# Optimization experiments

Measured on AMD Instinct MI355X. Metric: run time of the kernel, lower is better.

Reference implementation:

```python
import jax, jax.numpy as jnp
import numpy as np

N, C_IN, C_OUT, T, V = 64, 64, 64, 300, 25


def setup_inputs() -> dict:
    key = jax.random.key(0)
    k1, k2, k3, k4 = jax.random.split(key, 4)
    x = jax.random.normal(k1, (N, C_IN, T, V), dtype=jnp.float32)
    a = jax.random.uniform(k2, (N, T, V, V), dtype=jnp.float32)
    # 1x1 Conv2D (channels_first) == per-pixel channel-mixing matmul
    W = jax.random.normal(k3, (C_IN, C_OUT), dtype=jnp.float32) * (1.0 / np.sqrt(C_IN))
    b = jax.random.normal(k4, (C_OUT,), dtype=jnp.float32) * 0.01
    return {"x": x, "a": a, "W": W, "b": b}


def reference(x, a, W, b):
    # 1x1 conv channels_first: mix channels at every (t, v) location
    y = jnp.einsum('nctv,cd->ndtv', x, W) + b[None, :, None, None]
    # dropout in eval mode (training=False) is identity
    # spatial graph convolution: node mixing with per-(n,t) adjacency
    out = jnp.einsum('nctv,ntvw->nctw', y, a)
    return (out, a)
```

## Files before the change

kernel.cpp:

```cpp
#include <hip/hip_runtime.h>


typedef __attribute__((ext_vector_type(8))) short short8;
typedef __attribute__((ext_vector_type(4))) float f32x4;

#define XS_S 66
#define YS_S 36
#define AT_S 36

__device__ __forceinline__ unsigned short f2bf(float f) {
    unsigned int u = __builtin_bit_cast(unsigned int, f);
    return (unsigned short)((u + 0x7FFFu + ((u >> 16) & 1u)) >> 16);
}

__global__ __launch_bounds__(512, 6)
void sgcn_fused(const float* __restrict__ xg, const float* __restrict__ ag,
                const float* __restrict__ Wg, const float* __restrict__ bg,
                float* __restrict__ outg)
{
    __shared__ alignas(16) unsigned short Wt[64 * XS_S];
    __shared__ alignas(16) unsigned short Xs[4][32 * XS_S];
    __shared__ alignas(16) unsigned short Ys[8][32 * YS_S];
    __shared__ alignas(16) unsigned short At[4][32 * AT_S];

    const int tid  = threadIdx.x;
    const int wid  = tid >> 6;
    const int lane = tid & 63;
    const int q    = lane >> 4;
    const int lo   = lane & 15;

    const int bid = blockIdx.x;
    const int n   = bid / 75;
    const int t0  = (bid % 75) * 4;

    f32x4 xv[4];
    const long xbase = ((long)n * 64 * 300 + t0) * 25;
#pragma unroll
    for (int m = 0; m < 4; ++m) {
        const int f = tid + 512 * m;
        if (m < 3 || f < 1600) {
            const int c = f / 25, j = f % 25;
            xv[m] = *(const f32x4*)(xg + xbase + (long)c * 7500 + 4 * j);
        }
    }
    f32x4 av[2];
    const long abase = ((long)n * 300 + t0) * 625;
#pragma unroll
    for (int m = 0; m < 2; ++m) {
        const int f = tid + 512 * m;
        if (m < 1 || f < 625)
            av[m] = *(const f32x4*)(ag + abase + 4 * f);
    }
    f32x4 wv[2];
#pragma unroll
    for (int m = 0; m < 2; ++m)
        wv[m] = *(const f32x4*)(Wg + 4 * (tid + 512 * m));

    if (tid < 256) {
        unsigned short* yr = &Ys[tid >> 5][(tid & 31) * YS_S];
#pragma unroll
        for (int i = 25; i < 32; ++i) yr[i] = 0;
    } else if (tid < 384) {
        const int r = tid - 256;
        unsigned short* ar = &At[r >> 5][(r & 31) * AT_S];
#pragma unroll
        for (int i = 25; i < 32; ++i) ar[i] = 0;
    }

#pragma unroll
    for (int m = 0; m < 2; ++m) {
        const int f = 4 * (tid + 512 * m);
#pragma unroll
        for (int i = 0; i < 4; ++i) {
            const int e = f + i, c = e >> 6, d = e & 63;
            Wt[d * XS_S + c] = f2bf(wv[m][i]);
        }
    }
#pragma unroll
    for (int m = 0; m < 4; ++m) {
        const int f = tid + 512 * m;
        if (m < 3 || f < 1600) {
            const int c = f / 25, j = f % 25;
#pragma unroll
            for (int i = 0; i < 4; ++i) {
                const int e = 4 * j + i;
                const int tl = e / 25, v = e % 25;
                Xs[tl][v * XS_S + c] = f2bf(xv[m][i]);
            }
        }
    }
    {
        float* aout = outg + 30720000L + abase;
#pragma unroll
        for (int m = 0; m < 2; ++m) {
            const int f = tid + 512 * m;
            if (m < 1 || f < 625) {
                *(f32x4*)(aout + 4 * f) = av[m];
#pragma unroll
                for (int i = 0; i < 4; ++i) {
                    const int e = 4 * f + i;
                    const int tl = e / 625, r = e % 625;
                    At[tl][(r % 25) * AT_S + (r / 25)] = f2bf(av[m][i]);
                }
            }
        }
    }
    __syncthreads();

    const int tl = wid >> 1;
    const int dh = wid & 1;
    const int t  = t0 + tl;
    const int d0 = 32 * dh;

    short8 wfrag[2][2];
#pragma unroll
    for (int mi = 0; mi < 2; ++mi)
#pragma unroll
        for (int ki = 0; ki < 2; ++ki)
            wfrag[mi][ki] = *(const short8*)&Wt[(d0 + 16 * mi + lo) * XS_S + 32 * ki + 8 * q];

    f32x4 bias[2];
#pragma unroll
    for (int mi = 0; mi < 2; ++mi)
#pragma unroll
        for (int r = 0; r < 4; ++r)
            bias[mi][r] = bg[d0 + 16 * mi + 4 * q + r];

    unsigned short* xs = Xs[tl];
    unsigned short* ys = Ys[wid];
    unsigned short* at = At[tl];

    f32x4 accy[2][2];
#pragma unroll
    for (int mi = 0; mi < 2; ++mi) { accy[mi][0] = bias[mi]; accy[mi][1] = bias[mi]; }
#pragma unroll
    for (int ni = 0; ni < 2; ++ni)
#pragma unroll
        for (int ki = 0; ki < 2; ++ki) {
            const short8 bf = *(const short8*)&xs[(16 * ni + lo) * XS_S + 32 * ki + 8 * q];
#pragma unroll
            for (int mi = 0; mi < 2; ++mi)
                accy[mi][ni] = __builtin_amdgcn_mfma_f32_16x16x32_bf16(
                    wfrag[mi][ki], bf, accy[mi][ni], 0, 0, 0);
        }

#pragma unroll
    for (int mi = 0; mi < 2; ++mi)
#pragma unroll
        for (int ni = 0; ni < 2; ++ni) {
            const int v = 16 * ni + lo;
            if (v < 25) {
#pragma unroll
                for (int r = 0; r < 4; ++r)
                    ys[(16 * mi + 4 * q + r) * YS_S + v] = f2bf(accy[mi][ni][r]);
            }
        }

    short8 afr[2];
#pragma unroll
    for (int mi = 0; mi < 2; ++mi)
        afr[mi] = *(const short8*)&at[(16 * mi + lo) * AT_S + 8 * q];
    short8 yfr[2];
#pragma unroll
    for (int dj = 0; dj < 2; ++dj)
        yfr[dj] = *(const short8*)&ys[(16 * dj + lo) * YS_S + 8 * q];

    f32x4 acco[2][2];
#pragma unroll
    for (int mi = 0; mi < 2; ++mi)
#pragma unroll
        for (int dj = 0; dj < 2; ++dj)
            acco[mi][dj] = f32x4{0.f, 0.f, 0.f, 0.f};
#pragma unroll
    for (int mi = 0; mi < 2; ++mi)
#pragma unroll
        for (int dj = 0; dj < 2; ++dj)
            acco[mi][dj] = __builtin_amdgcn_mfma_f32_16x16x32_bf16(
                afr[mi], yfr[dj], acco[mi][dj], 0, 0, 0);

    float* op = outg + ((long)n * 64 * 300 + t) * 25;
#pragma unroll
    for (int dj = 0; dj < 2; ++dj) {
        const long dbase = (long)(d0 + 16 * dj + lo) * 7500;
        *(f32x4*)(op + dbase + 4 * q) = acco[0][dj];
        if (q < 2)
            *(f32x4*)(op + dbase + 16 + 4 * q) = acco[1][dj];
        else if (q == 2)
            op[dbase + 24] = acco[1][dj][0];
    }
}

extern "C" void kernel_launch(void* const* d_in, const int* in_sizes, int n_in,
                              void* d_out, int out_size, void* d_ws, size_t ws_size,
                              hipStream_t stream) {
    const float* x = (const float*)d_in[0];
    const float* a = (const float*)d_in[1];
    const float* W = (const float*)d_in[2];
    const float* b = (const float*)d_in[3];
    float* out = (float*)d_out;
    hipLaunchKernelGGL(sgcn_fused, dim3(64 * 75), dim3(512), 0, stream,
                       x, a, W, b, out);
}
```

Baseline: 76.90 us.

## Alias X and Y LDS buffers, load W fragments directly from global to raise occupancy

Removes the shared W transpose buffer by having each lane build its bf16 weight fragments straight from global memory (cached reads). X staging and the per-wave Y buffers now share a single LDS region, separated by an extra barrier, and padding zeros for Y are written during the Y store. The aim is a smaller LDS footprint so that 8 blocks per CU fit, with launch bounds raised to match. In exchange it adds a second __syncthreads and scalar, strided global reads of W per lane.

```diff
diff --git a/kernel.cpp b/kernel.cpp
--- a/kernel.cpp
+++ b/kernel.cpp
@@ -13,15 +13,13 @@
     return (unsigned short)((u + 0x7FFFu + ((u >> 16) & 1u)) >> 16);
 }
 
-__global__ __launch_bounds__(512, 6)
+__global__ __launch_bounds__(512, 8)
 void sgcn_fused(const float* __restrict__ xg, const float* __restrict__ ag,
                 const float* __restrict__ Wg, const float* __restrict__ bg,
                 float* __restrict__ outg)
 {
-    __shared__ alignas(16) unsigned short Wt[64 * XS_S];
-    __shared__ alignas(16) unsigned short Xs[4][32 * XS_S];
-    __shared__ alignas(16) unsigned short Ys[8][32 * YS_S];
-    __shared__ alignas(16) unsigned short At[4][32 * AT_S];
+    __shared__ alignas(16) unsigned short Ubuf[9216];
+    __shared__ alignas(16) unsigned short At[4 * 32 * AT_S];
 
     const int tid  = threadIdx.x;
     const int wid  = tid >> 6;
@@ -51,41 +49,26 @@
         if (m < 1 || f < 625)
             av[m] = *(const f32x4*)(ag + abase + 4 * f);
     }
-    f32x4 wv[2];
-#pragma unroll
-    for (int m = 0; m < 2; ++m)
-        wv[m] = *(const f32x4*)(Wg + 4 * (tid + 512 * m));
 
-    if (tid < 256) {
-        unsigned short* yr = &Ys[tid >> 5][(tid & 31) * YS_S];
-#pragma unroll
-        for (int i = 25; i < 32; ++i) yr[i] = 0;
-    } else if (tid < 384) {
-        const int r = tid - 256;
-        unsigned short* ar = &At[r >> 5][(r & 31) * AT_S];
+    if (tid < 128) {
+        unsigned short* ar = &At[(tid >> 5) * 32 * AT_S + (tid & 31) * AT_S];
 #pragma unroll
         for (int i = 25; i < 32; ++i) ar[i] = 0;
     }
 
+    {
+        unsigned short* Xs0 = Ubuf;
 #pragma unroll
-    for (int m = 0; m < 2; ++m) {
-        const int f = 4 * (tid + 512 * m);
+        for (int m = 0; m < 4; ++m) {
+            const int f = tid + 512 * m;
+            if (m < 3 || f < 1600) {
+                const int c = f / 25, j = f % 25;
 #pragma unroll
-        for (int i = 0; i < 4; ++i) {
-            const int e = f + i, c = e >> 6, d = e & 63;
-            Wt[d * XS_S + c] = f2bf(wv[m][i]);
-        }
-    }
-#pragma unroll
-    for (int m = 0; m < 4; ++m) {
-        const int f = tid + 512 * m;
-        if (m < 3 || f < 1600) {
-            const int c = f / 25, j = f % 25;
-#pragma unroll
-            for (int i = 0; i < 4; ++i) {
-                const int e = 4 * j + i;
-                const int tl = e / 25, v = e % 25;
-                Xs[tl][v * XS_S + c] = f2bf(xv[m][i]);
+                for (int i = 0; i < 4; ++i) {
+                    const int e = 4 * j + i;
+                    const int tl = e / 25, v = e % 25;
+                    Xs0[tl * (32 * XS_S) + v * XS_S + c] = f2bf(xv[m][i]);
+                }
             }
         }
     }
@@ -100,12 +83,11 @@
                 for (int i = 0; i < 4; ++i) {
                     const int e = 4 * f + i;
                     const int tl = e / 625, r = e % 625;
-                    At[tl][(r % 25) * AT_S + (r / 25)] = f2bf(av[m][i]);
+                    At[tl * (32 * AT_S) + (r % 25) * AT_S + (r / 25)] = f2bf(av[m][i]);
                 }
             }
         }
     }
-    __syncthreads();
 
     const int tl = wid >> 1;
     const int dh = wid & 1;
@@ -116,8 +98,14 @@
 #pragma unroll
     for (int mi = 0; mi < 2; ++mi)
 #pragma unroll
-        for (int ki = 0; ki < 2; ++ki)
-            wfrag[mi][ki] = *(const short8*)&Wt[(d0 + 16 * mi + lo) * XS_S + 32 * ki + 8 * q];
+        for (int ki = 0; ki < 2; ++ki) {
+            const int d = d0 + 16 * mi + lo;
+#pragma unroll
+            for (int i = 0; i < 8; ++i) {
+                const int c = 32 * ki + 8 * q + i;
+                wfrag[mi][ki][i] = (short)f2bf(Wg[c * 64 + d]);
+            }
+        }
 
     f32x4 bias[2];
 #pragma unroll
@@ -126,9 +114,9 @@
         for (int r = 0; r < 4; ++r)
             bias[mi][r] = bg[d0 + 16 * mi + 4 * q + r];
 
-    unsigned short* xs = Xs[tl];
-    unsigned short* ys = Ys[wid];
-    unsigned short* at = At[tl];
+    __syncthreads();
+
+    const unsigned short* xs = Ubuf + tl * (32 * XS_S);
 
     f32x4 accy[2][2];
 #pragma unroll
@@ -144,18 +132,22 @@
                     wfrag[mi][ki], bf, accy[mi][ni], 0, 0, 0);
         }
 
+    __syncthreads();
+
+    unsigned short* ys = Ubuf + wid * (32 * YS_S);
 #pragma unroll
     for (int mi = 0; mi < 2; ++mi)
 #pragma unroll
         for (int ni = 0; ni < 2; ++ni) {
             const int v = 16 * ni + lo;
-            if (v < 25) {
+            const bool ok = (v < 25);
 #pragma unroll
-                for (int r = 0; r < 4; ++r)
-                    ys[(16 * mi + 4 * q + r) * YS_S + v] = f2bf(accy[mi][ni][r]);
-            }
+            for (int r = 0; r < 4; ++r)
+                ys[(16 * mi + 4 * q + r) * YS_S + v] =
+                    ok ? f2bf(accy[mi][ni][r]) : (unsigned short)0;
         }
 
+    const unsigned short* at = At + tl * (32 * AT_S);
     short8 afr[2];
 #pragma unroll
     for (int mi = 0; mi < 2; ++mi)
```

New measurement: 101.5 us. 32.0% more time.
